# Kernel tuning notes

Hardware: AMD Instinct MI355X
Metric: run time of the kernel (lower is better)

The kernel has to match this reference:

```python
import jax, jax.numpy as jnp
import numpy as np


def setup_inputs() -> dict:
    key = jax.random.key(0)
    ks = jax.random.split(key, 6)
    B, Lq, Lm, D = 4, 2048, 2048, 1024
    s = D ** -0.5
    return {
        "input": jax.random.normal(ks[0], (B, Lq, D), jnp.float32),
        "memory": jax.random.normal(ks[1], (B, Lm, D), jnp.float32),
        # torch Linear weights are [out_features, in_features]
        "Wq": jax.random.normal(ks[2], (D, D), jnp.float32) * s,
        "Wk": jax.random.normal(ks[3], (D, D), jnp.float32) * s,
        "Wv": jax.random.normal(ks[4], (D, D), jnp.float32) * s,
        "Wo": jax.random.normal(ks[5], (D, D), jnp.float32) * s,
    }


def reference(input, memory, Wq, Wk, Wv, Wo):
    # q/k/v projections (Linear, no bias): x @ W.T
    depth = Wq.shape[0]
    q = jnp.einsum("bqd,ed->bqe", input, Wq) * (depth ** -0.5)
    k = jnp.einsum("bmd,ed->bme", memory, Wk)
    v = jnp.einsum("bmd,ed->bme", memory, Wv)
    logit = jnp.einsum("bqe,bme->bqm", q, k)          # [B, Lq, Lm]
    attention_weight = jax.nn.softmax(logit, axis=-1)
    attention_output = jnp.einsum("bqm,bme->bqe", attention_weight, v)
    return jnp.einsum("bqe,oe->bqo", attention_output, Wo)
```

## Files before the change

### kernel.cpp

```cpp
#include <hip/hip_runtime.h>
#include <hip/hip_bf16.h>

typedef unsigned short u16;
typedef __bf16 bf16x8 __attribute__((ext_vector_type(8)));
typedef float floatx4 __attribute__((ext_vector_type(4)));
typedef __hip_bfloat16 bf;

__device__ __forceinline__ __bf16 f2b(float f) {
    __hip_bfloat16 h = __float2bfloat16(f);
    return *reinterpret_cast<__bf16*>(&h);
}
__device__ __forceinline__ bf16x8 ld8f(const float* p) {
    float4 a = ((const float4*)p)[0];
    float4 b = ((const float4*)p)[1];
    bf16x8 r;
    r[0] = f2b(a.x); r[1] = f2b(a.y); r[2] = f2b(a.z); r[3] = f2b(a.w);
    r[4] = f2b(b.x); r[5] = f2b(b.y); r[6] = f2b(b.z); r[7] = f2b(b.w);
    return r;
}
__device__ __forceinline__ void storev(float* p, float v) { *p = v; }
__device__ __forceinline__ void storev(bf* p, float v)    { *p = __float2bfloat16(v); }

__device__ __forceinline__ void gl16(const bf* g, u16* l) {
    __builtin_amdgcn_global_load_lds(
        (const __attribute__((address_space(1))) void*)g,
        (__attribute__((address_space(3))) void*)l, 16, 0, 0);
}


#define FENCE asm volatile("" ::: "memory")
#define BARx  __builtin_amdgcn_s_barrier()
#define LGKM0 asm volatile("s_waitcnt lgkmcnt(0)" ::: "memory")
#define VM4   asm volatile("s_waitcnt vmcnt(4)" ::: "memory")
#define VM0   asm volatile("s_waitcnt vmcnt(0)" ::: "memory")

#define ST_A(h, kt, Ab) \
    gl16(Asrc + (long)((h) * 32) * K + (long)(kt) * 64, (Ab) + (h) * 4096 + tid * 8)
#define ST_B(c, kt, Bb) do { \
    gl16(Bsrc + (long)((c) * 32) * K + (long)(kt) * 64, (Bb) + (c) * 8192 + tid * 8); \
    gl16(Bsrc + (long)((c) * 32 + 128) * K + (long)(kt) * 64, (Bb) + (c) * 8192 + 4096 + tid * 8); \
} while (0)

#define RD_A(dst, h, Ab) do { _Pragma("unroll") \
    for (int q_ = 0; q_ < 2; q_++) { \
        const u16* p_ = (Ab) + ((h) * 64 + wg * 32 + q_ * 16 + fr) * 64; \
        dst[q_ * 2 + 0] = *(const bf16x8*)(p_ + kl0); \
        dst[q_ * 2 + 1] = *(const bf16x8*)(p_ + kl1); \
    } } while (0)

#define RD_B(dst, c, Bb) do { _Pragma("unroll") \
    for (int j_ = 0; j_ < 2; j_++) { \
        const u16* p_ = (Bb) + ((c) * 128 + w4 * 32 + j_ * 16 + fr) * 64; \
        dst[j_ * 2 + 0] = *(const bf16x8*)(p_ + kl0); \
        dst[j_ * 2 + 1] = *(const bf16x8*)(p_ + kl1); \
    } } while (0)

#define QMM(h, c, av, bv) do { _Pragma("unroll") \
    for (int q_ = 0; q_ < 2; q_++) _Pragma("unroll") \
    for (int j_ = 0; j_ < 2; j_++) _Pragma("unroll") \
    for (int kk_ = 0; kk_ < 2; kk_++) \
        acc[(h) * 2 + q_][(c) * 2 + j_] = __builtin_amdgcn_mfma_f32_16x16x32_bf16( \
            av[q_ * 2 + kk_], bv[j_ * 2 + kk_], acc[(h) * 2 + q_][(c) * 2 + j_], 0, 0, 0); \
} while (0)

template <typename OutT>
__device__ __forceinline__ void gemm8_core(
    const bf* __restrict__ A, const bf* __restrict__ B, OutT* __restrict__ C,
    int K, int N, int m_blk, int n_blk, float scale, u16* lds)
{
    const int tid  = threadIdx.x;
    const int w    = tid >> 6, lane = tid & 63;
    const int wg   = w >> 2, w4 = w & 3;
    const int fr   = lane & 15, kg = lane >> 4;

    u16* const A0b = lds;
    u16* const B0b = lds + 8192;
    u16* const A1b = lds + 24576;
    u16* const B1b = lds + 32768;

    const int kl0 = (kg * 8) ^ ((fr & 7) << 3);
    const int kl1 = kl0 ^ 32;

    const int sr  = tid >> 3;
    const int scs = ((tid & 7) * 8) ^ ((sr & 7) << 3);
    const bf* Asrc = A + (long)(m_blk + (tid >> 8) * 64 + (sr & 31)) * K + scs;
    const bf* Bsrc = B + (long)(n_blk + (tid >> 8) * 64 + (sr & 31)) * K + scs;

    floatx4 acc[4][4];
#pragma unroll
    for (int i = 0; i < 4; i++)
#pragma unroll
        for (int j = 0; j < 4; j++) acc[i][j] = (floatx4){0.f, 0.f, 0.f, 0.f};

    bf16x8 a0[4], a1[4], b0a[4], b0b[4], b1[4];

    const int T     = K >> 6;
    const int iters = T >> 1;

    ST_B(0, 0, B0b); ST_A(0, 0, A0b); ST_B(1, 0, B0b); ST_A(1, 0, A0b);
    ST_B(0, 1, B1b); ST_A(0, 1, A1b); ST_B(1, 1, B1b); ST_A(1, 1, A1b);
    VM0; BARx;
    RD_B(b0a, 0, B0b);
    LGKM0; BARx;

    for (int it = 0; it < iters; ++it) {
        const int t   = it * 2;
        const int ts0 = (t + 2 < T) ? t + 2 : 0;
        const int ts1 = (t + 3 < T) ? t + 3 : 0;

        RD_A(a0, 0, A0b);  ST_B(0, ts0, B0b);  FENCE; BARx; LGKM0;
        __builtin_amdgcn_s_setprio(1);
        if (it) QMM(1, 0, a1, b0b);
        __builtin_amdgcn_s_setprio(0);
        FENCE; BARx;

        RD_B(b1, 1, B0b);  ST_A(0, ts0, A0b);  FENCE; BARx; LGKM0;
        __builtin_amdgcn_s_setprio(1); QMM(0, 0, a0, b0a);
        __builtin_amdgcn_s_setprio(0); FENCE; BARx;

        RD_A(a1, 1, A0b);  ST_B(1, ts0, B0b);  FENCE; BARx; LGKM0;
        __builtin_amdgcn_s_setprio(1); QMM(0, 1, a0, b1);
        __builtin_amdgcn_s_setprio(0); FENCE; BARx;

        RD_B(b0b, 0, B1b); ST_A(1, ts0, A0b);  FENCE; BARx; LGKM0;
        __builtin_amdgcn_s_setprio(1); QMM(1, 1, a1, b1);
        __builtin_amdgcn_s_setprio(0); VM4; FENCE; BARx;

        RD_A(a0, 0, A1b);  ST_B(0, ts1, B1b);  FENCE; BARx; LGKM0;
        __builtin_amdgcn_s_setprio(1); QMM(1, 0, a1, b0a);
        __builtin_amdgcn_s_setprio(0); FENCE; BARx;

        RD_B(b1, 1, B1b);  ST_A(0, ts1, A1b);  FENCE; BARx; LGKM0;
        __builtin_amdgcn_s_setprio(1); QMM(0, 0, a0, b0b);
        __builtin_amdgcn_s_setprio(0); FENCE; BARx;

        RD_A(a1, 1, A1b);  ST_B(1, ts1, B1b);  FENCE; BARx; LGKM0;
        __builtin_amdgcn_s_setprio(1); QMM(0, 1, a0, b1);
        __builtin_amdgcn_s_setprio(0); FENCE; BARx;

        RD_B(b0a, 0, B0b); ST_A(1, ts1, A1b);  FENCE; BARx; LGKM0;
        __builtin_amdgcn_s_setprio(1); QMM(1, 1, a1, b1);
        __builtin_amdgcn_s_setprio(0); VM4; FENCE; BARx;
    }
    QMM(1, 0, a1, b0b);

    const long c_col0 = n_blk + w4 * 64 + fr;
    const long c_row0 = m_blk + wg * 64 + (lane >> 4) * 4;
#pragma unroll
    for (int rf = 0; rf < 4; rf++)
#pragma unroll
        for (int r = 0; r < 4; r++) {
            const long row = c_row0 + rf * 16 + r;
#pragma unroll
            for (int cf = 0; cf < 4; cf++)
                storev(&C[row * N + c_col0 + cf * 16], acc[rf][cf][r] * scale);
        }
}

template <typename OutT>
__global__ __launch_bounds__(512)
void gemm8(const bf* __restrict__ A, const bf* __restrict__ B,
           OutT* __restrict__ C, int K, int N,
           long sA, long sB, long sC, float scale)
{
    __shared__ __align__(16) u16 lds[49152];
    gemm8_core(A + blockIdx.z * sA, B + blockIdx.z * sB, C + blockIdx.z * sC,
               K, N, blockIdx.y * 128, blockIdx.x * 256, scale, lds);
}

__global__ __launch_bounds__(512)
void gemm8_qk(const bf* __restrict__ xb, const bf* __restrict__ memb,
              const bf* __restrict__ Wqb, const bf* __restrict__ Wkb,
              bf* __restrict__ Q, bf* __restrict__ Kp, float qscale)
{
    __shared__ __align__(16) u16 lds[49152];
    const int z = blockIdx.z;
    gemm8_core(z ? memb : xb, z ? Wkb : Wqb, z ? Kp : Q, 1024, 1024,
               blockIdx.y * 128, blockIdx.x * 256, z ? 1.f : qscale, lds);
}

__global__ __launch_bounds__(256)
void cvt2(const float* __restrict__ a, const float* __restrict__ b,
          bf* __restrict__ da, bf* __restrict__ db, long n)
{
    const float* s = blockIdx.z ? b : a;
    bf* d = blockIdx.z ? db : da;
    const long stride = (long)gridDim.x * 256;
    for (long i = (long)blockIdx.x * 256 + threadIdx.x; i * 8 < n; i += stride)
        *(bf16x8*)(d + i * 8) = ld8f(s + i * 8);
}

__global__ __launch_bounds__(256)
void cvt_w(const float* __restrict__ w0, const float* __restrict__ w1,
           const float* __restrict__ w2, const float* __restrict__ w3,
           bf* __restrict__ d)
{
    const int z = blockIdx.z;
    const float* s = (z == 0) ? w0 : (z == 1) ? w1 : (z == 2) ? w2 : w3;
    bf* dz = d + (long)z * (1 << 20);
    const long i = ((long)blockIdx.x * 256 + threadIdx.x) * 8;
    *(bf16x8*)(dz + i) = ld8f(s + i);
}

__global__ __launch_bounds__(256)
void softmax_rows_2048(bf* __restrict__ X)
{
    const long row = blockIdx.x;
    const int t = threadIdx.x;
    const int wave = t >> 6, lane = t & 63;
    __shared__ float red[8];

    float v[8];
    float m = -1e30f;
#pragma unroll
    for (int i = 0; i < 8; i++) {
        v[i] = __bfloat162float(X[row * 2048 + t + i * 256]);
        m = fmaxf(m, v[i]);
    }
#pragma unroll
    for (int o = 32; o > 0; o >>= 1) m = fmaxf(m, __shfl_xor(m, o, 64));
    if (lane == 0) red[wave] = m;
    __syncthreads();
    m = fmaxf(fmaxf(red[0], red[1]), fmaxf(red[2], red[3]));

    float s = 0.f;
#pragma unroll
    for (int i = 0; i < 8; i++) { v[i] = __expf(v[i] - m); s += v[i]; }
#pragma unroll
    for (int o = 32; o > 0; o >>= 1) s += __shfl_xor(s, o, 64);
    if (lane == 0) red[4 + wave] = s;
    __syncthreads();
    s = red[4] + red[5] + red[6] + red[7];

    const float inv = 1.f / s;
#pragma unroll
    for (int i = 0; i < 8; i++)
        X[row * 2048 + t + i * 256] = __float2bfloat16(v[i] * inv);
}

extern "C" void kernel_launch(void* const* d_in, const int* in_sizes, int n_in,
                              void* d_out, int out_size, void* d_ws, size_t ws_size,
                              hipStream_t stream)
{
    const float* x   = (const float*)d_in[0];
    const float* mem = (const float*)d_in[1];
    const float* Wq  = (const float*)d_in[2];
    const float* Wk  = (const float*)d_in[3];
    const float* Wv  = (const float*)d_in[4];
    const float* Wo  = (const float*)d_in[5];

    constexpr int  B = 4, L = 2048, D = 1024;
    constexpr long LD = (long)L * D;
    constexpr long LL = (long)L * L;
    constexpr size_t CH = 1u << 24;

    char* ws = (char*)d_ws;
    bf* Q   = (bf*)(ws + 0 * CH);
    bf* Kp  = (bf*)(ws + 1 * CH);
    bf* Vt  = (bf*)(ws + 2 * CH);
    bf* Wb  = (bf*)(ws + 3 * CH);
    bf* Wqb = Wb;
    bf* Wkb = Wb + (long)(1 << 20);
    bf* Wvb = Wb + (long)2 * (1 << 20);
    bf* Wob = Wb + (long)3 * (1 << 20);
    bf* AO  = Q;

    bf* xb   = (bf*)d_out;
    bf* memb = (bf*)d_out + B * LD;
    bf* Lg   = (bf*)d_out;

    const float qscale = 0.03125f;

    cvt2<<<dim3(1024, 1, 2), dim3(256), 0, stream>>>(x, mem, xb, memb, B * LD);
    cvt_w<<<dim3(512, 1, 4), dim3(256), 0, stream>>>(Wq, Wk, Wv, Wo, Wb);

    gemm8_qk<<<dim3(4, 64, 2), dim3(512), 0, stream>>>(
        xb, memb, Wqb, Wkb, Q, Kp, qscale);

    gemm8<bf><<<dim3(8, 8, 4), dim3(512), 0, stream>>>(
        Wvb, memb, Vt, D, L, 0, LD, (long)D * L, 1.f);

    gemm8<bf><<<dim3(8, 16, 4), dim3(512), 0, stream>>>(
        Q, Kp, Lg, D, L, LD, LD, LL, 1.f);

    softmax_rows_2048<<<dim3(B * L), dim3(256), 0, stream>>>(Lg);

    gemm8<bf><<<dim3(4, 16, 4), dim3(512), 0, stream>>>(
        Lg, Vt, AO, L, D, LL, (long)D * L, LD, 1.f);

    gemm8<float><<<dim3(4, 64, 1), dim3(512), 0, stream>>>(
        AO, Wob, (float*)d_out, D, D, 0, 0, 0, 1.f);
}
```

Before: 293.9 us.

## Restructure GEMM main loop into four phases with split B loads

Reworks the double-buffered bf16 GEMM main loop from eight barrier-separated phases into four. Each phase now reads both A halves and one B quarter, then issues two quadrant MFMAs, while the global-to-LDS loads for B are split into single-load pieces and redistributed across phases. The aim is fewer barriers per K-step, better balance of load issue, and dropping the peeled tail MFMA. In exchange, more fragment registers are live at once, and the new vmcnt(3) waits and the cross-phase load ordering need to be exactly right or stale LDS data could be read.

```diff
diff --git a/kernel.cpp b/kernel.cpp
--- a/kernel.cpp
+++ b/kernel.cpp
@@ -31,15 +31,15 @@
 #define FENCE asm volatile("" ::: "memory")
 #define BARx  __builtin_amdgcn_s_barrier()
 #define LGKM0 asm volatile("s_waitcnt lgkmcnt(0)" ::: "memory")
-#define VM4   asm volatile("s_waitcnt vmcnt(4)" ::: "memory")
+#define VM3   asm volatile("s_waitcnt vmcnt(3)" ::: "memory")
 #define VM0   asm volatile("s_waitcnt vmcnt(0)" ::: "memory")
 
 #define ST_A(h, kt, Ab) \
     gl16(Asrc + (long)((h) * 32) * K + (long)(kt) * 64, (Ab) + (h) * 4096 + tid * 8)
-#define ST_B(c, kt, Bb) do { \
-    gl16(Bsrc + (long)((c) * 32) * K + (long)(kt) * 64, (Bb) + (c) * 8192 + tid * 8); \
-    gl16(Bsrc + (long)((c) * 32 + 128) * K + (long)(kt) * 64, (Bb) + (c) * 8192 + 4096 + tid * 8); \
-} while (0)
+#define ST_Bu0(c, kt, Bb) \
+    gl16(Bsrc + (long)((c) * 32) * K + (long)(kt) * 64, (Bb) + (c) * 8192 + tid * 8)
+#define ST_Bu1(c, kt, Bb) \
+    gl16(Bsrc + (long)((c) * 32 + 128) * K + (long)(kt) * 64, (Bb) + (c) * 8192 + 4096 + tid * 8)
 
 #define RD_A(dst, h, Ab) do { _Pragma("unroll") \
     for (int q_ = 0; q_ < 2; q_++) { \
@@ -92,57 +92,46 @@
 #pragma unroll
         for (int j = 0; j < 4; j++) acc[i][j] = (floatx4){0.f, 0.f, 0.f, 0.f};
 
-    bf16x8 a0[4], a1[4], b0a[4], b0b[4], b1[4];
+    bf16x8 a0[4], a1[4], b0[4], b1[4];
 
     const int T     = K >> 6;
     const int iters = T >> 1;
 
-    ST_B(0, 0, B0b); ST_A(0, 0, A0b); ST_B(1, 0, B0b); ST_A(1, 0, A0b);
-    ST_B(0, 1, B1b); ST_A(0, 1, A1b); ST_B(1, 1, B1b); ST_A(1, 1, A1b);
+    ST_A(0, 0, A0b); ST_A(1, 0, A0b);
+    ST_Bu0(0, 0, B0b); ST_Bu1(0, 0, B0b); ST_Bu0(1, 0, B0b); ST_Bu1(1, 0, B0b);
+    ST_A(0, 1, A1b); ST_A(1, 1, A1b);
+    ST_Bu0(0, 1, B1b); ST_Bu1(0, 1, B1b); ST_Bu0(1, 1, B1b); ST_Bu1(1, 1, B1b);
     VM0; BARx;
-    RD_B(b0a, 0, B0b);
-    LGKM0; BARx;
 
     for (int it = 0; it < iters; ++it) {
         const int t   = it * 2;
         const int ts0 = (t + 2 < T) ? t + 2 : 0;
         const int ts1 = (t + 3 < T) ? t + 3 : 0;
 
-        RD_A(a0, 0, A0b);  ST_B(0, ts0, B0b);  FENCE; BARx; LGKM0;
-        __builtin_amdgcn_s_setprio(1);
-        if (it) QMM(1, 0, a1, b0b);
-        __builtin_amdgcn_s_setprio(0);
-        FENCE; BARx;
-
-        RD_B(b1, 1, B0b);  ST_A(0, ts0, A0b);  FENCE; BARx; LGKM0;
-        __builtin_amdgcn_s_setprio(1); QMM(0, 0, a0, b0a);
+        RD_A(a0, 0, A0b); RD_A(a1, 1, A0b); RD_B(b0, 0, B0b);
+        if (it) { ST_Bu1(0, t + 1, B1b); ST_Bu0(1, t + 1, B1b); ST_Bu1(1, t + 1, B1b); }
+        FENCE; BARx; LGKM0;
+        __builtin_amdgcn_s_setprio(1); QMM(0, 0, a0, b0); QMM(1, 0, a1, b0);
         __builtin_amdgcn_s_setprio(0); FENCE; BARx;
 
-        RD_A(a1, 1, A0b);  ST_B(1, ts0, B0b);  FENCE; BARx; LGKM0;
-        __builtin_amdgcn_s_setprio(1); QMM(0, 1, a0, b1);
+        RD_B(b1, 1, B0b);
+        ST_A(0, ts0, A0b); ST_A(1, ts0, A0b); ST_Bu0(0, ts0, B0b);
+        FENCE; BARx; LGKM0;
+        __builtin_amdgcn_s_setprio(1); QMM(0, 1, a0, b1); QMM(1, 1, a1, b1);
+        __builtin_amdgcn_s_setprio(0); VM3; FENCE; BARx;
+
+        RD_A(a0, 0, A1b); RD_A(a1, 1, A1b); RD_B(b0, 0, B1b);
+        ST_Bu1(0, ts0, B0b); ST_Bu0(1, ts0, B0b); ST_Bu1(1, ts0, B0b);
+        FENCE; BARx; LGKM0;
+        __builtin_amdgcn_s_setprio(1); QMM(0, 0, a0, b0); QMM(1, 0, a1, b0);
         __builtin_amdgcn_s_setprio(0); FENCE; BARx;
 
-        RD_B(b0b, 0, B1b); ST_A(1, ts0, A0b);  FENCE; BARx; LGKM0;
-        __builtin_amdgcn_s_setprio(1); QMM(1, 1, a1, b1);
-        __builtin_amdgcn_s_setprio(0); VM4; FENCE; BARx;
-
-        RD_A(a0, 0, A1b);  ST_B(0, ts1, B1b);  FENCE; BARx; LGKM0;
-        __builtin_amdgcn_s_setprio(1); QMM(1, 0, a1, b0a);
-        __builtin_amdgcn_s_setprio(0); FENCE; BARx;
-
-        RD_B(b1, 1, B1b);  ST_A(0, ts1, A1b);  FENCE; BARx; LGKM0;
-        __builtin_amdgcn_s_setprio(1); QMM(0, 0, a0, b0b);
-        __builtin_amdgcn_s_setprio(0); FENCE; BARx;
-
-        RD_A(a1, 1, A1b);  ST_B(1, ts1, B1b);  FENCE; BARx; LGKM0;
-        __builtin_amdgcn_s_setprio(1); QMM(0, 1, a0, b1);
-        __builtin_amdgcn_s_setprio(0); FENCE; BARx;
-
-        RD_B(b0a, 0, B0b); ST_A(1, ts1, A1b);  FENCE; BARx; LGKM0;
-        __builtin_amdgcn_s_setprio(1); QMM(1, 1, a1, b1);
-        __builtin_amdgcn_s_setprio(0); VM4; FENCE; BARx;
+        RD_B(b1, 1, B1b);
+        ST_A(0, ts1, A1b); ST_A(1, ts1, A1b); ST_Bu0(0, ts1, B1b);
+        FENCE; BARx; LGKM0;
+        __builtin_amdgcn_s_setprio(1); QMM(0, 1, a0, b1); QMM(1, 1, a1, b1);
+        __builtin_amdgcn_s_setprio(0); VM3; FENCE; BARx;
     }
-    QMM(1, 0, a1, b0b);
 
     const long c_col0 = n_blk + w4 * 64 + fr;
     const long c_row0 = m_blk + wg * 64 + (lane >> 4) * 4;
```

After: 300.4 us. 1.02x slower.
